# Performance work log

Hardware: AMD Instinct MI355X
Metric: run time of the kernel (lower is better)

Reference implementation:

```python
import jax, jax.numpy as jnp
import numpy as np

# Poincare ball hyperbolic multi-head attention (hypll-style HMultiheadAttention)
C = 1.0          # ball curvature
SQRT_C = 1.0
EPS = 1e-7
B, S, E, H = 4, 1024, 512, 8
HD = E // H      # head_dim = 64


def _project_to_ball(u, scale=0.5):
    n = jnp.linalg.norm(u, axis=-1, keepdims=True)
    return u * (scale / (1.0 + n))  # guarantees ||x|| < scale < 1/sqrt(C)


def h_linear(x, z, r):
    """Poincare fully-connected layer (Shimizu et al. HNN++), as in hypll HLinear.
    x: [..., n] points in the ball, z: [n, m] weight directions, r: [m] bias."""
    x2 = jnp.sum(x * x, -1, keepdims=True)
    lam = 2.0 / jnp.maximum(1.0 - C * x2, EPS)          # conformal factor lambda_x
    zn = jnp.maximum(jnp.linalg.norm(z, axis=0), EPS)    # [m]
    xz = x @ z                                           # [..., m]
    two_cr = 2.0 * SQRT_C * r
    v = (2.0 * zn / SQRT_C) * jnp.arcsinh(
        SQRT_C * lam * xz / zn * jnp.cosh(two_cr) - (lam - 1.0) * jnp.sinh(two_cr)
    )
    v2 = jnp.sum(v * v, -1, keepdims=True)
    return v / (1.0 + jnp.sqrt(1.0 + C * v2))            # map back into the ball


def _split_heads(x):
    b, s, e = x.shape
    return x.reshape(b, s, H, HD).transpose(0, 2, 1, 3)  # [B,H,S,hd]; matches split(dim=-1)


def _h_attention(q, k, v):
    # similarity = -poincare_dist(q, k), pairwise via the arccosh closed form
    # (avoids materializing a [B,H,Sq,Sk,hd] mobius_add tensor)
    q2 = jnp.sum(q * q, -1)[..., :, None]                # [B,H,Sq,1]
    k2 = jnp.sum(k * k, -1)[..., None, :]                # [B,H,1,Sk]
    qk = jnp.einsum('bhqd,bhkd->bhqk', q, k)
    diff2 = jnp.maximum(q2 + k2 - 2.0 * qk, 0.0)
    denom = jnp.maximum((1.0 - C * q2) * (1.0 - C * k2), EPS)
    arg = 1.0 + 2.0 * C * diff2 / denom
    dist = jnp.arccosh(jnp.maximum(arg, 1.0 + EPS)) / SQRT_C
    w = jax.nn.softmax(-dist, axis=-1)                   # attention_activation
    # attention_midpoint: weighted Mobius gyromidpoint then half scalar-mul
    v2 = jnp.sum(v * v, -1)                              # [B,H,Sk]
    lam = 2.0 / jnp.maximum(1.0 - C * v2, EPS)
    num = jnp.einsum('bhqk,bhkd->bhqd', w * lam[..., None, :], v)
    den = jnp.einsum('bhqk,bhk->bhq', w, lam - 1.0)[..., None]
    m_bar = num / jnp.where(jnp.abs(den) < EPS, EPS, den)
    mn = jnp.maximum(jnp.linalg.norm(m_bar, axis=-1, keepdims=True), EPS)
    t = jnp.minimum(SQRT_C * mn, 1.0 - 1e-6)
    return jnp.tanh(0.5 * jnp.arctanh(t)) * m_bar / (SQRT_C * mn)  # (1/2) mobius-scalar-mul


def setup_inputs() -> dict:
    key = jax.random.key(0)
    ks = jax.random.split(key, 9)
    query = _project_to_ball(jax.random.normal(ks[0], (B, S, E), jnp.float32))
    key_t = _project_to_ball(jax.random.normal(ks[1], (B, S, E), jnp.float32))
    value = _project_to_ball(jax.random.normal(ks[2], (B, S, E), jnp.float32))
    scale = E ** -0.5
    zq = jax.random.normal(ks[3], (E, E), jnp.float32) * scale
    zk = jax.random.normal(ks[4], (E, E), jnp.float32) * scale
    zv = jax.random.normal(ks[5], (E, E), jnp.float32) * scale
    rq = jax.random.normal(ks[6], (E,), jnp.float32) * 0.01
    rk = jax.random.normal(ks[7], (E,), jnp.float32) * 0.01
    rv = jax.random.normal(ks[8], (E,), jnp.float32) * 0.01
    return {"query": query, "key": key_t, "value": value,
            "zq": zq, "rq": rq, "zk": zk, "rk": rk, "zv": zv, "rv": rv}


def reference(query, key, value, zq, rq, zk, rk, zv, rv):
    pq = h_linear(query, zq, rq)
    pk = h_linear(key, zk, rk)
    pv = h_linear(value, zv, rv)
    q, k, v = _split_heads(pq), _split_heads(pk), _split_heads(pv)
    out = _h_attention(q, k, v)                          # [B,H,S,hd]
    return out.transpose(0, 2, 1, 3).reshape(B, S, E)    # manifold.cat over heads
```

## Files before the change

### kernel.cpp

```cpp
#include <hip/hip_runtime.h>
#include <hip/hip_bf16.h>
#include <math.h>

#define EPSf 1e-7f
typedef unsigned short u16;
typedef __attribute__((ext_vector_type(8))) short bf16x8;
typedef __attribute__((ext_vector_type(4))) float f32x4;

__device__ __forceinline__ float bf2f(u16 u) {
  union { unsigned int i; float f; } x; x.i = ((unsigned int)u) << 16; return x.f;
}
__device__ __forceinline__ u16 f2bf(float f) {
  union { float f; unsigned int i; } x; x.f = f;
  unsigned int r = x.i + 0x7fffu + ((x.i >> 16) & 1u);
  return (u16)(r >> 16);
}
__device__ __forceinline__ void gll16(const void* g, void* l) {
  __builtin_amdgcn_global_load_lds((__attribute__((address_space(1))) void*)(g),
                                   (__attribute__((address_space(3))) void*)(l),
                                   16, 0, 0);
}

__global__ __launch_bounds__(256) void split_x(
    const float* __restrict__ xq, const float* __restrict__ xk, const float* __restrict__ xv,
    u16* __restrict__ Xh, u16* __restrict__ Xl,
    float* __restrict__ Xn, float* __restrict__ Vn, float* __restrict__ Zn) {
  if (blockIdx.x == 0) {
    #pragma unroll
    for (int j = 0; j < 6; ++j) Zn[threadIdx.x + 256 * j] = 0.f;
  }
  const int gr = blockIdx.x * 2 + (threadIdx.x >> 7);
  const int mat = gr >> 12, row = gr & 4095;
  const float* X = (mat == 0) ? xq : (mat == 1) ? xk : xv;
  const int f4 = threadIdx.x & 127;
  float4 x = ((const float4*)(X + (size_t)row * 512))[f4];
  u16 h0 = f2bf(x.x), h1 = f2bf(x.y), h2 = f2bf(x.z), h3 = f2bf(x.w);
  u16 l0 = f2bf(x.x - bf2f(h0)), l1 = f2bf(x.y - bf2f(h1));
  u16 l2 = f2bf(x.z - bf2f(h2)), l3 = f2bf(x.w - bf2f(h3));
  ((ushort4*)(Xh + (size_t)gr * 512))[f4] = make_ushort4(h0, h1, h2, h3);
  ((ushort4*)(Xl + (size_t)gr * 512))[f4] = make_ushort4(l0, l1, l2, l3);
  float a = fmaf(x.x, x.x, fmaf(x.y, x.y, fmaf(x.z, x.z, x.w * x.w)));
  a += __shfl_xor(a, 1);  a += __shfl_xor(a, 2);  a += __shfl_xor(a, 4);
  a += __shfl_xor(a, 8);  a += __shfl_xor(a, 16); a += __shfl_xor(a, 32);
  __shared__ float red[4];
  if ((threadIdx.x & 63) == 0) red[threadIdx.x >> 6] = a;
  __syncthreads();
  if (threadIdx.x == 0)   { Xn[gr] = red[0] + red[1]; Vn[gr] = 0.f; }
  if (threadIdx.x == 128) { Xn[gr] = red[2] + red[3]; Vn[gr] = 0.f; }
}

__global__ __launch_bounds__(256) void split_z(
    const float* __restrict__ zq, const float* __restrict__ zk, const float* __restrict__ zv,
    u16* __restrict__ ZhT, u16* __restrict__ ZlT, float* __restrict__ Zn) {
  const int idx = blockIdx.x;
  const int mat = idx >> 6;
  const int cg = (idx >> 3) & 7, kt = idx & 7;
  const int c0 = cg * 64;
  const float* Z = (mat == 0) ? zq : (mat == 1) ? zk : zv;
  __shared__ float tile[64][68];
  const int t = threadIdx.x;
  {
    int kl = t >> 2;
    const float* src = Z + (size_t)(kt * 64 + kl) * 512 + c0 + (t & 3) * 16;
    #pragma unroll
    for (int j = 0; j < 4; ++j) {
      float4 v = *(const float4*)(src + 4 * j);
      *(float4*)&tile[kl][(t & 3) * 16 + 4 * j] = v;
    }
  }
  __syncthreads();
  const int cl = t >> 2, kg4 = t & 3;
  const size_t zo = (size_t)mat * 512 * 512;
  float csum = 0.f;
  #pragma unroll
  for (int jj = 0; jj < 4; ++jj) {
    u16 hb[4], lb[4];
    #pragma unroll
    for (int qq = 0; qq < 4; ++qq) {
      float zval = tile[kg4 * 16 + jj * 4 + qq][cl];
      csum = fmaf(zval, zval, csum);
      u16 hh = f2bf(zval);
      hb[qq] = hh;
      lb[qq] = f2bf(zval - bf2f(hh));
    }
    size_t o = zo + (size_t)(c0 + cl) * 512 + kt * 64 + kg4 * 16 + jj * 4;
    *(ushort4*)(ZhT + o) = make_ushort4(hb[0], hb[1], hb[2], hb[3]);
    *(ushort4*)(ZlT + o) = make_ushort4(lb[0], lb[1], lb[2], lb[3]);
  }
  csum += __shfl_xor(csum, 1);
  csum += __shfl_xor(csum, 2);
  if (kg4 == 0) atomicAdd(&Zn[mat * 512 + c0 + cl], csum);
}

__global__ __launch_bounds__(256) void proj_gemm(
    const u16* __restrict__ Xh, const u16* __restrict__ Xl,
    const u16* __restrict__ ZhT, const u16* __restrict__ ZlT,
    const float* __restrict__ Xn, const float* __restrict__ Zn,
    const float* __restrict__ rq, const float* __restrict__ rk, const float* __restrict__ rv,
    float* __restrict__ Vtmp, float* __restrict__ Vn) {
  const int m0 = blockIdx.x * 64;
  const int n0 = blockIdx.y * 128;
  const int mat = blockIdx.z;
  const size_t xoff = (size_t)mat * 4096 * 512;
  const size_t zoff = (size_t)mat * 512 * 512;
  const int t = threadIdx.x, wv = t >> 6, lane = t & 63;
  const int l15 = lane & 15, quad = lane >> 4;
  const int wm = wv >> 1, wn = wv & 1;

  __shared__ __align__(16) u16 SM[12288];
  __shared__ float lams[64], lam1s[64], wmxs[128], wmys[128], wmzs[128];

  if (t < 64) {
    float x2 = Xn[mat * 4096 + m0 + t];
    float lam = 2.f / fmaxf(1.f - x2, EPSf);
    lams[t] = lam; lam1s[t] = lam - 1.f;
  }
  if (t < 128) {
    float zn = fmaxf(sqrtf(Zn[mat * 512 + n0 + t]), EPSf);
    const float* R = (mat == 0) ? rq : (mat == 1) ? rk : rv;
    float tr = 2.f * R[n0 + t];
    float e = expf(tr), ei = 1.f / e;
    wmxs[t] = 0.5f * (e + ei) / zn;
    wmys[t] = 0.5f * (e - ei);
    wmzs[t] = 2.f * zn;
  }

  f32x4 acc[2][4];
  #pragma unroll
  for (int i = 0; i < 2; ++i)
    #pragma unroll
    for (int j = 0; j < 4; ++j) acc[i][j] = (f32x4){0.f, 0.f, 0.f, 0.f};

  const u16* gs[6];
  u16* ld[6];
  #pragma unroll
  for (int ci = 0; ci < 6; ++ci) {
    int c = wv + 4 * ci;
    const u16* arr; int row0, lo;
    if (c < 4)       { arr = Xh + xoff;  row0 = m0 + 16 * c;        lo = c * 512; }
    else if (c < 8)  { arr = Xl + xoff;  row0 = m0 + 16 * (c - 4);  lo = 2048 + (c - 4) * 512; }
    else if (c < 16) { arr = ZhT + zoff; row0 = n0 + 16 * (c - 8);  lo = 4096 + (c - 8) * 512; }
    else             { arr = ZlT + zoff; row0 = n0 + 16 * (c - 16); lo = 8192 + (c - 16) * 512; }
    gs[ci] = arr + (size_t)(row0 + (lane >> 2)) * 512 + (lane & 3) * 8;
    ld[ci] = SM + lo;
  }

  for (int k0 = 0; k0 < 512; k0 += 32) {
    __syncthreads();
    #pragma unroll
    for (int ci = 0; ci < 6; ++ci) gll16(gs[ci] + k0, ld[ci]);
    __syncthreads();
    bf16x8 ah[2], al[2], bh_[4], bl_[4];
    #pragma unroll
    for (int i = 0; i < 2; ++i) {
      int ra = wm * 32 + i * 16 + l15;
      ah[i] = *(const bf16x8*)&SM[ra * 32 + quad * 8];
      al[i] = *(const bf16x8*)&SM[2048 + ra * 32 + quad * 8];
    }
    #pragma unroll
    for (int j = 0; j < 4; ++j) {
      int rb = wn * 64 + j * 16 + l15;
      bh_[j] = *(const bf16x8*)&SM[4096 + rb * 32 + quad * 8];
      bl_[j] = *(const bf16x8*)&SM[8192 + rb * 32 + quad * 8];
    }
    #pragma unroll
    for (int i = 0; i < 2; ++i)
      #pragma unroll
      for (int j = 0; j < 4; ++j) {
        acc[i][j] = __builtin_amdgcn_mfma_f32_16x16x32_bf16(ah[i], bh_[j], acc[i][j], 0, 0, 0);
        acc[i][j] = __builtin_amdgcn_mfma_f32_16x16x32_bf16(ah[i], bl_[j], acc[i][j], 0, 0, 0);
        acc[i][j] = __builtin_amdgcn_mfma_f32_16x16x32_bf16(al[i], bh_[j], acc[i][j], 0, 0, 0);
      }
  }

  #pragma unroll
  for (int i = 0; i < 2; ++i) {
    float rsum[4] = {0.f, 0.f, 0.f, 0.f};
    #pragma unroll
    for (int j = 0; j < 4; ++j) {
      int nl = wn * 64 + j * 16 + l15;
      float wx = wmxs[nl], wy = wmys[nl], wz = wmzs[nl];
      #pragma unroll
      for (int r = 0; r < 4; ++r) {
        int ml = wm * 32 + i * 16 + quad * 4 + r;
        float tt = lams[ml] * acc[i][j][r] * wx - lam1s[ml] * wy;
        float v = wz * logf(tt + sqrtf(fmaf(tt, tt, 1.f)));
        Vtmp[xoff + (size_t)(m0 + ml) * 512 + (n0 + nl)] = v;
        rsum[r] = fmaf(v, v, rsum[r]);
      }
    }
    #pragma unroll
    for (int r = 0; r < 4; ++r) {
      rsum[r] += __shfl_xor(rsum[r], 1);
      rsum[r] += __shfl_xor(rsum[r], 2);
      rsum[r] += __shfl_xor(rsum[r], 4);
      rsum[r] += __shfl_xor(rsum[r], 8);
    }
    if (l15 == 0) {
      #pragma unroll
      for (int r = 0; r < 4; ++r)
        atomicAdd(&Vn[mat * 4096 + m0 + wm * 32 + i * 16 + quad * 4 + r], rsum[r]);
    }
  }
}

__global__ __launch_bounds__(256) void pack(
    const float* __restrict__ Vtmp, const float* __restrict__ Vn,
    u16* __restrict__ Qh, u16* __restrict__ Kh, u16* __restrict__ VTb,
    float* __restrict__ q2a, float* __restrict__ aqa, float4* __restrict__ ksc) {
  __shared__ u16 tile[64][72];
  __shared__ float lams[64];
  const int t = threadIdx.x;
  if (blockIdx.x < 256) {
    const int mat = blockIdx.x >> 7;
    const int rb = blockIdx.x & 127;
    const int r = t >> 3, h = t & 7;
    const int row = rb * 32 + r;
    const size_t gr = (size_t)mat * 4096 + row;
    const float sc = 1.f / (1.f + sqrtf(1.f + Vn[gr]));
    const float* src = Vtmp + gr * 512 + h * 64;
    const int b = row >> 10, s = row & 1023;
    u16* dst = (mat ? Kh : Qh) + ((size_t)(b * 8 + h) * 1024 + s) * 64;
    float nrm = 0.f;
    #pragma unroll
    for (int j = 0; j < 16; ++j) {
      float4 x = *(const float4*)(src + 4 * j);
      u16 u0 = f2bf(x.x * sc), u1 = f2bf(x.y * sc), u2 = f2bf(x.z * sc), u3 = f2bf(x.w * sc);
      *(ushort4*)(dst + 4 * j) = make_ushort4(u0, u1, u2, u3);
      float f0 = bf2f(u0), f1 = bf2f(u1), f2 = bf2f(u2), f3 = bf2f(u3);
      nrm += f0 * f0 + f1 * f1 + f2 * f2 + f3 * f3;
    }
    const size_t so = (size_t)(b * 8 + h) * 1024 + s;
    if (mat == 0) { q2a[so] = nrm; aqa[so] = 1.f / fmaxf(1.f - nrm, EPSf); }
    else {
      float2 kk = make_float2(nrm, 2.f / fmaxf(1.f - nrm, EPSf));
      *(float2*)&ksc[so] = kk;
    }
  } else {
    const int idx = blockIdx.x - 256;
    const int bh = idx >> 4, st = idx & 15;
    const int b = bh >> 3, h = bh & 7;
    {
      const int s = t >> 2, dg = t & 3;
      const size_t gr = (size_t)2 * 4096 + b * 1024 + st * 64 + s;
      const float sc = 1.f / (1.f + sqrtf(1.f + Vn[gr]));
      const float* src = Vtmp + gr * 512 + h * 64 + dg * 16;
      float nrm = 0.f;
      #pragma unroll
      for (int j = 0; j < 4; ++j) {
        float4 x = *(const float4*)(src + 4 * j);
        u16 u0 = f2bf(x.x * sc), u1 = f2bf(x.y * sc), u2 = f2bf(x.z * sc), u3 = f2bf(x.w * sc);
        *(ushort4*)&tile[s][dg * 16 + 4 * j] = make_ushort4(u0, u1, u2, u3);
        float f0 = bf2f(u0), f1 = bf2f(u1), f2 = bf2f(u2), f3 = bf2f(u3);
        nrm += f0 * f0 + f1 * f1 + f2 * f2 + f3 * f3;
      }
      nrm += __shfl_xor(nrm, 1);
      nrm += __shfl_xor(nrm, 2);
      if (dg == 0) {
        float lam = 2.f / fmaxf(1.f - nrm, EPSf);
        lams[s] = lam;
        ((float*)&ksc[(size_t)bh * 1024 + st * 64 + s])[3] = lam - 1.f;
      }
    }
    __syncthreads();
    const int d = t >> 2, sg = t & 3;
    u16 ob[16];
    #pragma unroll
    for (int j = 0; j < 16; ++j) {
      int ss = sg * 16 + j;
      ob[j] = f2bf(bf2f(tile[ss][d]) * lams[ss]);
    }
    u16* dst = VTb + ((size_t)bh * 64 + d) * 1024 + st * 64 + sg * 16;
    #pragma unroll
    for (int j = 0; j < 4; ++j)
      *(ushort4*)(dst + 4 * j) = make_ushort4(ob[4 * j], ob[4 * j + 1], ob[4 * j + 2], ob[4 * j + 3]);
  }
}

__global__ __launch_bounds__(256, 4) void attn(
    const u16* __restrict__ Qh, const u16* __restrict__ Kh, const u16* __restrict__ VTb,
    const float* __restrict__ q2a, const float* __restrict__ aqa,
    const float4* __restrict__ ksc, float* __restrict__ out) {
  const int bh = blockIdx.x;
  const int b = bh >> 3, h = bh & 7;
  const int q0 = blockIdx.y * 32;
  const int t = threadIdx.x, wv = t >> 6, lane = t & 63;
  const int l15 = lane & 15, quad = lane >> 4;
  const int kq = wv;

  __shared__ __align__(16) u16 Ws[4][32 * 72];
  __shared__ float k2s[4][64], cks[4][64], l1s[4][64];
  __shared__ __align__(16) float nums[2][32][68];
  __shared__ float dens[2][32];

  const size_t qkoff = (size_t)bh * 65536;

  bf16x8 qf[2][2];
  float q2r[2], aqr[2];
  #pragma unroll
  for (int qs = 0; qs < 2; ++qs) {
    int qrow = q0 + qs * 16 + l15;
    const u16* qp = Qh + qkoff + (size_t)qrow * 64 + quad * 8;
    qf[qs][0] = *(const bf16x8*)qp;
    qf[qs][1] = *(const bf16x8*)(qp + 32);
    q2r[qs] = q2a[bh * 1024 + qrow];
    aqr[qs] = aqa[bh * 1024 + qrow];
  }

  f32x4 num[2][4];
  #pragma unroll
  for (int qs = 0; qs < 2; ++qs)
    #pragma unroll
    for (int tm = 0; tm < 4; ++tm) num[qs][tm] = (f32x4){0.f, 0.f, 0.f, 0.f};
  float denp[2] = {0.f, 0.f};

  #pragma unroll 1
  for (int i = 0; i < 4; ++i) {
    const int ktc = kq + 4 * i;
    float4 scur = ksc[bh * 1024 + ktc * 64 + lane];
    bf16x8 kcur[8];
    #pragma unroll
    for (int tn = 0; tn < 4; ++tn)
      #pragma unroll
      for (int ks = 0; ks < 2; ++ks)
        kcur[tn * 2 + ks] = *(const bf16x8*)(Kh + qkoff +
            (size_t)(ktc * 64 + tn * 16 + l15) * 64 + ks * 32 + quad * 8);
    bf16x8 vf[8];
    #pragma unroll
    for (int tm = 0; tm < 4; ++tm)
      #pragma unroll
      for (int ks = 0; ks < 2; ++ks)
        vf[tm * 2 + ks] = *(const bf16x8*)(VTb + qkoff +
            (size_t)(tm * 16 + l15) * 1024 + ktc * 64 + ks * 32 + quad * 8);
    k2s[wv][lane] = scur.x;
    cks[wv][lane] = scur.y;
    l1s[wv][lane] = scur.w;

    #pragma unroll
    for (int tn = 0; tn < 4; ++tn) {
      const float4 k2v = *(const float4*)&k2s[wv][tn * 16 + quad * 4];
      const float4 ckv = *(const float4*)&cks[wv][tn * 16 + quad * 4];
      const float4 l1v = *(const float4*)&l1s[wv][tn * 16 + quad * 4];
      #pragma unroll
      for (int qs = 0; qs < 2; ++qs) {
        f32x4 s = (f32x4){0.f, 0.f, 0.f, 0.f};
        s = __builtin_amdgcn_mfma_f32_16x16x32_bf16(kcur[tn * 2 + 0], qf[qs][0], s, 0, 0, 0);
        s = __builtin_amdgcn_mfma_f32_16x16x32_bf16(kcur[tn * 2 + 1], qf[qs][1], s, 0, 0, 0);
        unsigned up[2];
        #pragma unroll
        for (int pr = 0; pr < 2; ++pr) {
          float w2[2];
          #pragma unroll
          for (int e = 0; e < 2; ++e) {
            const int r = pr * 2 + e;
            float d2 = fmaxf(fmaf(-2.f, s[r], q2r[qs] + ((const float*)&k2v)[r]), 0.f);
            float u = fmaxf(d2 * ((const float*)&ckv)[r] * aqr[qs], EPSf);
            w2[e] = (1.f + u) - sqrtf(fmaf(u, u, u + u));
          }
          union { __hip_bfloat162 h2; unsigned u; } cv;
          cv.h2 = __float22bfloat162_rn(make_float2(w2[0], w2[1]));
          up[pr] = cv.u;
          float wlo = __uint_as_float(cv.u << 16);
          float whi = __uint_as_float(cv.u & 0xffff0000u);
          denp[qs] = fmaf(wlo, ((const float*)&l1v)[pr * 2 + 0], denp[qs]);
          denp[qs] = fmaf(whi, ((const float*)&l1v)[pr * 2 + 1], denp[qs]);
        }
        *(uint2*)&Ws[wv][(qs * 16 + l15) * 72 + tn * 16 + quad * 4] = make_uint2(up[0], up[1]);
      }
    }
    #pragma unroll
    for (int qs = 0; qs < 2; ++qs)
      #pragma unroll
      for (int ks = 0; ks < 2; ++ks) {
        const bf16x8 wf = *(const bf16x8*)&Ws[wv][(qs * 16 + l15) * 72 + ks * 32 + quad * 8];
        #pragma unroll
        for (int tm = 0; tm < 4; ++tm)
          num[qs][tm] = __builtin_amdgcn_mfma_f32_16x16x32_bf16(
              vf[tm * 2 + ks], wf, num[qs][tm], 0, 0, 0);
      }
  }

  #pragma unroll
  for (int qs = 0; qs < 2; ++qs) {
    denp[qs] += __shfl_xor(denp[qs], 16);
    denp[qs] += __shfl_xor(denp[qs], 32);
  }

  if (wv & 1) {
    const int buf = wv >> 1;
    #pragma unroll
    for (int qs = 0; qs < 2; ++qs) {
      #pragma unroll
      for (int tm = 0; tm < 4; ++tm)
        *(float4*)&nums[buf][qs * 16 + l15][tm * 16 + quad * 4] =
            make_float4(num[qs][tm][0], num[qs][tm][1], num[qs][tm][2], num[qs][tm][3]);
      if (quad == 0) dens[buf][qs * 16 + l15] = denp[qs];
    }
  }
  __syncthreads();
  if (!(wv & 1)) {
    const int buf = wv >> 1;
    #pragma unroll
    for (int qs = 0; qs < 2; ++qs) {
      #pragma unroll
      for (int tm = 0; tm < 4; ++tm) {
        float4 o = *(const float4*)&nums[buf][qs * 16 + l15][tm * 16 + quad * 4];
        num[qs][tm][0] += o.x; num[qs][tm][1] += o.y;
        num[qs][tm][2] += o.z; num[qs][tm][3] += o.w;
      }
      denp[qs] += dens[buf][qs * 16 + l15];
    }
  }
  if (wv == 2) {
    #pragma unroll
    for (int qs = 0; qs < 2; ++qs) {
      #pragma unroll
      for (int tm = 0; tm < 4; ++tm)
        *(float4*)&nums[1][qs * 16 + l15][tm * 16 + quad * 4] =
            make_float4(num[qs][tm][0], num[qs][tm][1], num[qs][tm][2], num[qs][tm][3]);
      if (quad == 0) dens[1][qs * 16 + l15] = denp[qs];
    }
  }
  __syncthreads();
  if (wv == 0) {
    #pragma unroll
    for (int qs = 0; qs < 2; ++qs) {
      #pragma unroll
      for (int tm = 0; tm < 4; ++tm) {
        float4 o = *(const float4*)&nums[1][qs * 16 + l15][tm * 16 + quad * 4];
        num[qs][tm][0] += o.x; num[qs][tm][1] += o.y;
        num[qs][tm][2] += o.z; num[qs][tm][3] += o.w;
      }
      float den = denp[qs] + dens[1][qs * 16 + l15];
      den = (fabsf(den) < EPSf) ? EPSf : den;
      float inv = 1.f / den;
      float mv[4][4];
      float p = 0.f;
      #pragma unroll
      for (int tm = 0; tm < 4; ++tm) {
        mv[tm][0] = num[qs][tm][0] * inv;
        mv[tm][1] = num[qs][tm][1] * inv;
        mv[tm][2] = num[qs][tm][2] * inv;
        mv[tm][3] = num[qs][tm][3] * inv;
        p = fmaf(mv[tm][0], mv[tm][0], p); p = fmaf(mv[tm][1], mv[tm][1], p);
        p = fmaf(mv[tm][2], mv[tm][2], p); p = fmaf(mv[tm][3], mv[tm][3], p);
      }
      p += __shfl_xor(p, 16);
      p += __shfl_xor(p, 32);
      float mn = sqrtf(p);
      float mnc = fmaxf(mn, EPSf);
      float tt2 = fminf(mnc, 1.f - 1e-6f);
      float scale = tt2 / ((1.f + sqrtf(fmaxf(1.f - tt2 * tt2, 0.f))) * mnc);
      const size_t qg = (size_t)b * 1024 + q0 + qs * 16 + l15;
      #pragma unroll
      for (int tm = 0; tm < 4; ++tm) {
        float4 o = make_float4(mv[tm][0] * scale, mv[tm][1] * scale,
                               mv[tm][2] * scale, mv[tm][3] * scale);
        *(float4*)(out + qg * 512 + h * 64 + tm * 16 + quad * 4) = o;
      }
    }
  }
}

extern "C" void kernel_launch(void* const* d_in, const int* in_sizes, int n_in,
                              void* d_out, int out_size, void* d_ws, size_t ws_size,
                              hipStream_t stream) {
  (void)in_sizes; (void)n_in; (void)out_size; (void)ws_size;
  const float* q  = (const float*)d_in[0];
  const float* k  = (const float*)d_in[1];
  const float* v  = (const float*)d_in[2];
  const float* zq = (const float*)d_in[3];
  const float* rq = (const float*)d_in[4];
  const float* zk = (const float*)d_in[5];
  const float* rk = (const float*)d_in[6];
  const float* zv = (const float*)d_in[7];
  const float* rv = (const float*)d_in[8];

  unsigned char* ws = (unsigned char*)d_ws;
  u16*   Xh   = (u16*)(ws + 0);
  u16*   Xl   = (u16*)(ws + 12582912);
  u16*   ZhT  = (u16*)(ws + 25165824);
  u16*   ZlT  = (u16*)(ws + 26738688);
  float* Vtmp = (float*)(ws + 28311552);
  float* Xn   = (float*)(ws + 53477376);
  float* Vn   = (float*)(ws + 53526528);
  float* Zn   = (float*)(ws + 53575680);
  u16*   Qh   = (u16*)(ws + 0);
  u16*   Kh   = (u16*)(ws + 4194304);
  u16*   VTb  = (u16*)(ws + 8388608);
  float* q2a  = (float*)(ws + 12582912);
  float* aqa  = (float*)(ws + 12713984);
  float4* ksc = (float4*)(ws + 12845056);

  split_x<<<6144, 256, 0, stream>>>(q, k, v, Xh, Xl, Xn, Vn, Zn);
  split_z<<<192, 256, 0, stream>>>(zq, zk, zv, ZhT, ZlT, Zn);
  proj_gemm<<<dim3(64, 4, 3), 256, 0, stream>>>(Xh, Xl, ZhT, ZlT, Xn, Zn, rq, rk, rv, Vtmp, Vn);
  pack<<<768, 256, 0, stream>>>(Vtmp, Vn, Qh, Kh, VTb, q2a, aqa, ksc);
  attn<<<dim3(32, 32), 256, 0, stream>>>(Qh, Kh, VTb, q2a, aqa, ksc, (float*)d_out);
}
```

Before: 180.4 us.

## Merge split kernels into one launch, defer V loads, lower attn occupancy bound

Merges the split_x and split_z kernels into a single prep launch that branches on block index, and moves zeroing of Zn to a hipMemsetAsync. This removes one kernel boundary but adds a memset node. In attn, the V fragment loads now happen just before the PV MFMAs, one k-slice at a time, which cuts live registers. The launch bound changes from 4 to 3 waves per SIMD, giving the compiler more registers at the cost of occupancy.

```diff
diff --git a/kernel.cpp b/kernel.cpp
--- a/kernel.cpp
+++ b/kernel.cpp
@@ -21,75 +21,70 @@
                                    16, 0, 0);
 }
 
-__global__ __launch_bounds__(256) void split_x(
+__global__ __launch_bounds__(256) void prep(
     const float* __restrict__ xq, const float* __restrict__ xk, const float* __restrict__ xv,
+    const float* __restrict__ zq, const float* __restrict__ zk, const float* __restrict__ zv,
     u16* __restrict__ Xh, u16* __restrict__ Xl,
-    float* __restrict__ Xn, float* __restrict__ Vn, float* __restrict__ Zn) {
-  if (blockIdx.x == 0) {
-    #pragma unroll
-    for (int j = 0; j < 6; ++j) Zn[threadIdx.x + 256 * j] = 0.f;
-  }
-  const int gr = blockIdx.x * 2 + (threadIdx.x >> 7);
-  const int mat = gr >> 12, row = gr & 4095;
-  const float* X = (mat == 0) ? xq : (mat == 1) ? xk : xv;
-  const int f4 = threadIdx.x & 127;
-  float4 x = ((const float4*)(X + (size_t)row * 512))[f4];
-  u16 h0 = f2bf(x.x), h1 = f2bf(x.y), h2 = f2bf(x.z), h3 = f2bf(x.w);
-  u16 l0 = f2bf(x.x - bf2f(h0)), l1 = f2bf(x.y - bf2f(h1));
-  u16 l2 = f2bf(x.z - bf2f(h2)), l3 = f2bf(x.w - bf2f(h3));
-  ((ushort4*)(Xh + (size_t)gr * 512))[f4] = make_ushort4(h0, h1, h2, h3);
-  ((ushort4*)(Xl + (size_t)gr * 512))[f4] = make_ushort4(l0, l1, l2, l3);
-  float a = fmaf(x.x, x.x, fmaf(x.y, x.y, fmaf(x.z, x.z, x.w * x.w)));
-  a += __shfl_xor(a, 1);  a += __shfl_xor(a, 2);  a += __shfl_xor(a, 4);
-  a += __shfl_xor(a, 8);  a += __shfl_xor(a, 16); a += __shfl_xor(a, 32);
-  __shared__ float red[4];
-  if ((threadIdx.x & 63) == 0) red[threadIdx.x >> 6] = a;
-  __syncthreads();
-  if (threadIdx.x == 0)   { Xn[gr] = red[0] + red[1]; Vn[gr] = 0.f; }
-  if (threadIdx.x == 128) { Xn[gr] = red[2] + red[3]; Vn[gr] = 0.f; }
-}
-
-__global__ __launch_bounds__(256) void split_z(
-    const float* __restrict__ zq, const float* __restrict__ zk, const float* __restrict__ zv,
+    float* __restrict__ Xn, float* __restrict__ Vn,
     u16* __restrict__ ZhT, u16* __restrict__ ZlT, float* __restrict__ Zn) {
-  const int idx = blockIdx.x;
-  const int mat = idx >> 6;
-  const int cg = (idx >> 3) & 7, kt = idx & 7;
-  const int c0 = cg * 64;
-  const float* Z = (mat == 0) ? zq : (mat == 1) ? zk : zv;
   __shared__ float tile[64][68];
   const int t = threadIdx.x;
-  {
-    int kl = t >> 2;
-    const float* src = Z + (size_t)(kt * 64 + kl) * 512 + c0 + (t & 3) * 16;
-    #pragma unroll
-    for (int j = 0; j < 4; ++j) {
-      float4 v = *(const float4*)(src + 4 * j);
-      *(float4*)&tile[kl][(t & 3) * 16 + 4 * j] = v;
-    }
-  }
-  __syncthreads();
-  const int cl = t >> 2, kg4 = t & 3;
-  const size_t zo = (size_t)mat * 512 * 512;
-  float csum = 0.f;
-  #pragma unroll
-  for (int jj = 0; jj < 4; ++jj) {
-    u16 hb[4], lb[4];
-    #pragma unroll
-    for (int qq = 0; qq < 4; ++qq) {
-      float zval = tile[kg4 * 16 + jj * 4 + qq][cl];
-      csum = fmaf(zval, zval, csum);
-      u16 hh = f2bf(zval);
-      hb[qq] = hh;
-      lb[qq] = f2bf(zval - bf2f(hh));
-    }
-    size_t o = zo + (size_t)(c0 + cl) * 512 + kt * 64 + kg4 * 16 + jj * 4;
-    *(ushort4*)(ZhT + o) = make_ushort4(hb[0], hb[1], hb[2], hb[3]);
-    *(ushort4*)(ZlT + o) = make_ushort4(lb[0], lb[1], lb[2], lb[3]);
-  }
-  csum += __shfl_xor(csum, 1);
-  csum += __shfl_xor(csum, 2);
-  if (kg4 == 0) atomicAdd(&Zn[mat * 512 + c0 + cl], csum);
+  if (blockIdx.x < 6144) {
+    const int gr = blockIdx.x * 2 + (t >> 7);
+    const int mat = gr >> 12, row = gr & 4095;
+    const float* X = (mat == 0) ? xq : (mat == 1) ? xk : xv;
+    const int f4 = t & 127;
+    float4 x = ((const float4*)(X + (size_t)row * 512))[f4];
+    u16 h0 = f2bf(x.x), h1 = f2bf(x.y), h2 = f2bf(x.z), h3 = f2bf(x.w);
+    u16 l0 = f2bf(x.x - bf2f(h0)), l1 = f2bf(x.y - bf2f(h1));
+    u16 l2 = f2bf(x.z - bf2f(h2)), l3 = f2bf(x.w - bf2f(h3));
+    ((ushort4*)(Xh + (size_t)gr * 512))[f4] = make_ushort4(h0, h1, h2, h3);
+    ((ushort4*)(Xl + (size_t)gr * 512))[f4] = make_ushort4(l0, l1, l2, l3);
+    float a = fmaf(x.x, x.x, fmaf(x.y, x.y, fmaf(x.z, x.z, x.w * x.w)));
+    a += __shfl_xor(a, 1);  a += __shfl_xor(a, 2);  a += __shfl_xor(a, 4);
+    a += __shfl_xor(a, 8);  a += __shfl_xor(a, 16); a += __shfl_xor(a, 32);
+    if ((t & 63) == 0) tile[0][t >> 6] = a;
+    __syncthreads();
+    if (t == 0)   { Xn[gr] = tile[0][0] + tile[0][1]; Vn[gr] = 0.f; }
+    if (t == 128) { Xn[gr] = tile[0][2] + tile[0][3]; Vn[gr] = 0.f; }
+  } else {
+    const int idx = blockIdx.x - 6144;
+    const int mat = idx >> 6;
+    const int cg = (idx >> 3) & 7, kt = idx & 7;
+    const int c0 = cg * 64;
+    const float* Z = (mat == 0) ? zq : (mat == 1) ? zk : zv;
+    {
+      int kl = t >> 2;
+      const float* src = Z + (size_t)(kt * 64 + kl) * 512 + c0 + (t & 3) * 16;
+      #pragma unroll
+      for (int j = 0; j < 4; ++j) {
+        float4 v = *(const float4*)(src + 4 * j);
+        *(float4*)&tile[kl][(t & 3) * 16 + 4 * j] = v;
+      }
+    }
+    __syncthreads();
+    const int cl = t >> 2, kg4 = t & 3;
+    const size_t zo = (size_t)mat * 512 * 512;
+    float csum = 0.f;
+    #pragma unroll
+    for (int jj = 0; jj < 4; ++jj) {
+      u16 hb[4], lb[4];
+      #pragma unroll
+      for (int qq = 0; qq < 4; ++qq) {
+        float zval = tile[kg4 * 16 + jj * 4 + qq][cl];
+        csum = fmaf(zval, zval, csum);
+        u16 hh = f2bf(zval);
+        hb[qq] = hh;
+        lb[qq] = f2bf(zval - bf2f(hh));
+      }
+      size_t o = zo + (size_t)(c0 + cl) * 512 + kt * 64 + kg4 * 16 + jj * 4;
+      *(ushort4*)(ZhT + o) = make_ushort4(hb[0], hb[1], hb[2], hb[3]);
+      *(ushort4*)(ZlT + o) = make_ushort4(lb[0], lb[1], lb[2], lb[3]);
+    }
+    csum += __shfl_xor(csum, 1);
+    csum += __shfl_xor(csum, 2);
+    if (kg4 == 0) atomicAdd(&Zn[mat * 512 + c0 + cl], csum);
+  }
 }
 
 __global__ __launch_bounds__(256) void proj_gemm(
@@ -277,7 +272,7 @@
   }
 }
 
-__global__ __launch_bounds__(256, 4) void attn(
+__global__ __launch_bounds__(256, 3) void attn(
     const u16* __restrict__ Qh, const u16* __restrict__ Kh, const u16* __restrict__ VTb,
     const float* __restrict__ q2a, const float* __restrict__ aqa,
     const float4* __restrict__ ksc, float* __restrict__ out) {
@@ -325,13 +320,6 @@
       for (int ks = 0; ks < 2; ++ks)
         kcur[tn * 2 + ks] = *(const bf16x8*)(Kh + qkoff +
             (size_t)(ktc * 64 + tn * 16 + l15) * 64 + ks * 32 + quad * 8);
-    bf16x8 vf[8];
-    #pragma unroll
-    for (int tm = 0; tm < 4; ++tm)
-      #pragma unroll
-      for (int ks = 0; ks < 2; ++ks)
-        vf[tm * 2 + ks] = *(const bf16x8*)(VTb + qkoff +
-            (size_t)(tm * 16 + l15) * 1024 + ktc * 64 + ks * 32 + quad * 8);
     k2s[wv][lane] = scur.x;
     cks[wv][lane] = scur.y;
     l1s[wv][lane] = scur.w;
@@ -369,15 +357,21 @@
       }
     }
     #pragma unroll
-    for (int qs = 0; qs < 2; ++qs)
-      #pragma unroll
-      for (int ks = 0; ks < 2; ++ks) {
+    for (int ks = 0; ks < 2; ++ks) {
+      bf16x8 vfk[4];
+      #pragma unroll
+      for (int tm = 0; tm < 4; ++tm)
+        vfk[tm] = *(const bf16x8*)(VTb + qkoff +
+            (size_t)(tm * 16 + l15) * 1024 + ktc * 64 + ks * 32 + quad * 8);
+      #pragma unroll
+      for (int qs = 0; qs < 2; ++qs) {
         const bf16x8 wf = *(const bf16x8*)&Ws[wv][(qs * 16 + l15) * 72 + ks * 32 + quad * 8];
         #pragma unroll
         for (int tm = 0; tm < 4; ++tm)
           num[qs][tm] = __builtin_amdgcn_mfma_f32_16x16x32_bf16(
-              vf[tm * 2 + ks], wf, num[qs][tm], 0, 0, 0);
-      }
+              vfk[tm], wf, num[qs][tm], 0, 0, 0);
+      }
+    }
   }
 
   #pragma unroll
@@ -492,8 +486,8 @@
   float* aqa  = (float*)(ws + 12713984);
   float4* ksc = (float4*)(ws + 12845056);
 
-  split_x<<<6144, 256, 0, stream>>>(q, k, v, Xh, Xl, Xn, Vn, Zn);
-  split_z<<<192, 256, 0, stream>>>(zq, zk, zv, ZhT, ZlT, Zn);
+  hipMemsetAsync(Zn, 0, 6144, stream);
+  prep<<<6336, 256, 0, stream>>>(q, k, v, zq, zk, zv, Xh, Xl, Xn, Vn, ZhT, ZlT, Zn);
   proj_gemm<<<dim3(64, 4, 3), 256, 0, stream>>>(Xh, Xl, ZhT, ZlT, Xn, Zn, rq, rk, rv, Vtmp, Vn);
   pack<<<768, 256, 0, stream>>>(Vtmp, Vn, Qh, Kh, VTb, q2a, aqa, ksc);
   attn<<<dim3(32, 32), 256, 0, stream>>>(Qh, Kh, VTb, q2a, aqa, ksc, (float*)d_out);
```

After: 177.1 us. About the same (-1.8%).
